# Kernel optimization log

Measured on AMD Instinct MI355X. Metric: run time of the kernel, lower is better.

## Reference

```python
import jax, jax.numpy as jnp
import numpy as np

N = 50000
E = 800000
IN, HID, OUT = 20, 64, 2
HEADS, HD = 4, 64
EPS = 1e-5


def setup_inputs() -> dict:
    key = jax.random.key(0)
    ks = jax.random.split(key, 24)
    rn = lambda k, shape, s=0.1: (jax.random.normal(k, shape, dtype=jnp.float32) * s)
    inp = {}
    inp['x'] = jax.random.normal(ks[0], (N, IN), dtype=jnp.float32)
    inp['edge_index'] = jax.random.randint(ks[1], (2, E), 0, N, dtype=jnp.int64)
    # SAGEConv1: lin_l (aggregated msgs, bias), lin_r (root, no bias)
    inp['Wl1'] = rn(ks[2], (IN, HID)); inp['Wr1'] = rn(ks[3], (IN, HID)); inp['b1'] = jnp.zeros((HID,), jnp.float32)
    inp['g1'] = jnp.ones((HID,), jnp.float32); inp['bt1'] = jnp.zeros((HID,), jnp.float32)
    # GATConv: W2 projects to heads*dim; att vectors per head; bias size HID (concat=False)
    inp['W2'] = rn(ks[4], (HID, HEADS * HD)); inp['att_src'] = rn(ks[5], (HEADS, HD)); inp['att_dst'] = rn(ks[6], (HEADS, HD)); inp['b2'] = jnp.zeros((HID,), jnp.float32)
    inp['g2'] = jnp.ones((HID,), jnp.float32); inp['bt2'] = jnp.zeros((HID,), jnp.float32)
    # SAGEConv3: hidden -> hidden//2
    inp['Wl3'] = rn(ks[7], (HID, HID // 2)); inp['Wr3'] = rn(ks[8], (HID, HID // 2)); inp['b3'] = jnp.zeros((HID // 2,), jnp.float32)
    inp['g3'] = jnp.ones((HID // 2,), jnp.float32); inp['bt3'] = jnp.zeros((HID // 2,), jnp.float32)
    # skip + classifier
    inp['Wskip'] = rn(ks[9], (IN, HID // 2)); inp['bskip'] = jnp.zeros((HID // 2,), jnp.float32)
    inp['Wc1'] = rn(ks[10], (HID // 2, 32)); inp['bc1'] = jnp.zeros((32,), jnp.float32)
    inp['Wc2'] = rn(ks[11], (32, OUT)); inp['bc2'] = jnp.zeros((OUT,), jnp.float32)
    return inp


def _bn_eval(h, g, b):
    # eval-mode BatchNorm with freshly initialized running stats (mean=0, var=1)
    return h * (g / jnp.sqrt(1.0 + EPS)) + b


def reference(x, edge_index, Wl1, Wr1, b1, g1, bt1, W2, att_src, att_dst, b2, g2, bt2,
              Wl3, Wr3, b3, g3, bt3, Wskip, bskip, Wc1, bc1, Wc2, bc2):
    src, dst = edge_index[0], edge_index[1]
    deg = jnp.clip(jax.ops.segment_sum(jnp.ones((E,), x.dtype), dst, num_segments=N), 1.0)

    def sage(h, Wl, Wr, b):
        agg = jax.ops.segment_sum(h[src], dst, num_segments=N) / deg[:, None]  # mean aggregation
        return agg @ Wl + h @ Wr + b

    def gat(h):
        hp = (h @ W2).reshape(N, HEADS, HD)                    # [N,H,D]
        a_s = jnp.einsum('nhd,hd->nh', hp, att_src)            # [N,H]
        a_d = jnp.einsum('nhd,hd->nh', hp, att_dst)
        e = jax.nn.leaky_relu(a_s[src] + a_d[dst], 0.2)        # [E,H]
        m = jax.ops.segment_max(e, dst, num_segments=N)        # segment softmax over incoming edges
        ex = jnp.exp(e - m[dst])
        denom = jax.ops.segment_sum(ex, dst, num_segments=N)
        alpha = ex / (denom[dst] + 1e-16)                      # [E,H]
        out = jax.ops.segment_sum(hp[src] * alpha[:, :, None], dst, num_segments=N)  # [N,H,D]
        return out.mean(axis=1) + b2                            # concat=False -> mean over heads

    identity = x @ Wskip + bskip
    h = jax.nn.relu(_bn_eval(sage(x, Wl1, Wr1, b1), g1, bt1))   # dropout inactive (eval)
    h = jax.nn.relu(_bn_eval(gat(h), g2, bt2))
    h = jax.nn.relu(_bn_eval(sage(h, Wl3, Wr3, b3), g3, bt3))
    h = h + identity
    logits = jax.nn.relu(h @ Wc1 + bc1) @ Wc2 + bc2
    return jax.nn.log_softmax(logits, axis=1)
```

## Files before the change

kernel.cpp:

```cpp
#include <hip/hip_runtime.h>
#include <hip/hip_fp16.h>
#include <math.h>

#define NN 50000
#define NE 800000
#define IN_F 20
#define HID 64
#define HEADS 4
#define HD 64
#define CH 32
#define C1 32
#define OUTC 2

__global__ void k_scan_block(const int* __restrict__ in, int* __restrict__ out,
                             int* __restrict__ bsum, int n){
  __shared__ int tmp[256];
  int g = blockIdx.x * 256 + threadIdx.x;
  int v = (g < n) ? in[g] : 0;
  tmp[threadIdx.x] = v;
  __syncthreads();
  for (int o = 1; o < 256; o <<= 1) {
    int t = ((int)threadIdx.x >= o) ? tmp[threadIdx.x - o] : 0;
    __syncthreads();
    tmp[threadIdx.x] += t;
    __syncthreads();
  }
  if (g < n) out[g] = tmp[threadIdx.x] - v;
  if (bsum && threadIdx.x == 255) bsum[blockIdx.x] = tmp[255];
}

__global__ void k_add_off(int* __restrict__ rowptr, const int* __restrict__ bsum_ex, int n){
  int g = blockIdx.x * 256 + threadIdx.x;
  if (g < n) rowptr[g] += bsum_ex[g >> 8];
  if (g == 0) rowptr[NN] = NE;
}

__global__ void k_scatter(const int* __restrict__ src, const int* __restrict__ dst,
                          const int* __restrict__ rowptr, int* __restrict__ cnt2,
                          unsigned* __restrict__ colu){
  int e = blockIdx.x * 256 + threadIdx.x;
  if (e >= NE) return;
  int d = dst[e];
  int p = rowptr[d] + atomicAdd(&cnt2[d], 1);
  colu[p] = (unsigned)src[e] | ((unsigned)d << 16);
}

__global__ void k_prep(const float* __restrict__ x, const float* __restrict__ W2,
                       const float* __restrict__ att_src, const float* __restrict__ att_dst,
                       const int* __restrict__ dst,
                       __half* __restrict__ xh, float* __restrict__ was,
                       float* __restrict__ wad, float* __restrict__ W2r,
                       int* __restrict__ count){
  int i = blockIdx.x * 256 + threadIdx.x;
  if (i < NN * IN_F) xh[i] = __float2half(x[i]);
  if (i < NE) atomicAdd(&count[dst[i]], 1);
  if (i < 256 * 64) {
    int hk = i >> 6, d = i & 63;
    int h = hk >> 6, k = hk & 63;
    W2r[i] = W2[k * 256 + h * 64 + d];
  }
  if (i < 256) {
    int h = i >> 6, k = i & 63;
    float s = 0.f, dd = 0.f;
    for (int d = 0; d < 64; d++) {
      float w = W2[k * 256 + h * 64 + d];
      s  += w * att_src[h * 64 + d];
      dd += w * att_dst[h * 64 + d];
    }
    was[i] = s; wad[i] = dd;
  }
}

__global__ void k_aggx_gather(const int* __restrict__ rowptr, const unsigned* __restrict__ colu,
                              const __half* __restrict__ xh, float* __restrict__ aggx){
  int wid = threadIdx.x >> 6, lane = threadIdx.x & 63;
  int grp = lane >> 5, f = lane & 31;
  int n = blockIdx.x * 4 + wid;
  if (n >= NN) return;
  int r0 = rowptr[n], r1 = rowptr[n + 1];
  int ff = f < IN_F ? f : 0;
  float acc = 0.f;
  int base = r0;
  for (; base + 8 <= r1; base += 8) {
    int s0 = colu[base + grp] & 0xffff;
    int s1 = colu[base + 2 + grp] & 0xffff;
    int s2 = colu[base + 4 + grp] & 0xffff;
    int s3 = colu[base + 6 + grp] & 0xffff;
    float v0 = __half2float(xh[s0 * IN_F + ff]);
    float v1 = __half2float(xh[s1 * IN_F + ff]);
    float v2 = __half2float(xh[s2 * IN_F + ff]);
    float v3 = __half2float(xh[s3 * IN_F + ff]);
    acc += (v0 + v1) + (v2 + v3);
  }
  for (int j = base + grp; j < r1; j += 2)
    acc += __half2float(xh[(colu[j] & 0xffff) * IN_F + ff]);
  acc += __shfl_xor(acc, 32);
  if (grp == 0 && f < IN_F) aggx[n * IN_F + f] = acc;
}

__global__ void k_sage1(const float* __restrict__ x, const float* __restrict__ aggx,
                        const int* __restrict__ count,
                        const float* __restrict__ Wl, const float* __restrict__ Wr,
                        const float* __restrict__ b, const float* __restrict__ g,
                        const float* __restrict__ bt,
                        const float* __restrict__ was, const float* __restrict__ wad,
                        __half* __restrict__ h1h, float* __restrict__ a_s,
                        float* __restrict__ a_d){
  __shared__ float sWl[IN_F * HID], sWr[IN_F * HID], sWas[256], sWad[256];
  for (int i = threadIdx.x; i < IN_F * HID; i += 256) { sWl[i] = Wl[i]; sWr[i] = Wr[i]; }
  { int i = threadIdx.x; sWas[i] = was[i]; sWad[i] = wad[i]; }
  __syncthreads();
  int idx = blockIdx.x * 256 + threadIdx.x;
  if (idx >= NN * HID) return;
  int n = idx >> 6, j = idx & 63;
  float inv = 1.f / fmaxf((float)count[n], 1.f);
  const float* xr = x + n * IN_F;
  const float* ar = aggx + n * IN_F;
  float acc = b[j];
  #pragma unroll
  for (int k = 0; k < IN_F; k++)
    acc += (ar[k] * inv) * sWl[k * HID + j] + xr[k] * sWr[k * HID + j];
  acc = acc * (g[j] * rsqrtf(1.f + 1e-5f)) + bt[j];
  acc = fmaxf(acc, 0.f);
  h1h[idx] = __float2half(acc);
  #pragma unroll
  for (int h = 0; h < HEADS; h++) {
    float vs = acc * sWas[h * 64 + j];
    float vd = acc * sWad[h * 64 + j];
    #pragma unroll
    for (int o = 32; o > 0; o >>= 1) { vs += __shfl_down(vs, o); vd += __shfl_down(vd, o); }
    if (j == 0) { a_s[n * 4 + h] = vs; a_d[n * 4 + h] = vd; }
  }
}

static __device__ __forceinline__ float4 edge_p(float4 as, float4 ad){
  float e0 = as.x + ad.x; e0 = e0 >= 0.f ? e0 : 0.2f * e0;
  float e1 = as.y + ad.y; e1 = e1 >= 0.f ? e1 : 0.2f * e1;
  float e2 = as.z + ad.z; e2 = e2 >= 0.f ? e2 : 0.2f * e2;
  float e3 = as.w + ad.w; e3 = e3 >= 0.f ? e3 : 0.2f * e3;
  return make_float4(__expf(e0), __expf(e1), __expf(e2), __expf(e3));
}

__global__ void k_gat_fused(const int* __restrict__ rowptr, const unsigned* __restrict__ colu,
                            const float4* __restrict__ a_s4, const float4* __restrict__ a_d4,
                            const __half* __restrict__ h1h, __half* __restrict__ z){
  int wid = threadIdx.x >> 6;
  int lane = threadIdx.x & 63;
  int grp = lane >> 5;
  int idx = lane & 31;
  int n = blockIdx.x * 4 + wid;
  if (n >= NN) return;
  int r0 = rowptr[n], r1 = rowptr[n + 1];
  float4 ad = a_d4[n];
  float l0 = 0.f, l1 = 0.f, l2 = 0.f, l3 = 0.f;
  float2 ac0 = {0,0}, ac1 = {0,0}, ac2 = {0,0}, ac3 = {0,0};
  int base = r0;
  for (; base + 8 <= r1; base += 8) {
    int s0 = colu[base + grp] & 0xffff;
    int s1 = colu[base + 2 + grp] & 0xffff;
    int s2 = colu[base + 4 + grp] & 0xffff;
    int s3 = colu[base + 6 + grp] & 0xffff;
    float4 as0 = a_s4[s0], as1 = a_s4[s1], as2 = a_s4[s2], as3 = a_s4[s3];
    float2 v0 = __half22float2(*(const __half2*)(h1h + (size_t)s0 * 64 + 2 * idx));
    float2 v1 = __half22float2(*(const __half2*)(h1h + (size_t)s1 * 64 + 2 * idx));
    float2 v2 = __half22float2(*(const __half2*)(h1h + (size_t)s2 * 64 + 2 * idx));
    float2 v3 = __half22float2(*(const __half2*)(h1h + (size_t)s3 * 64 + 2 * idx));
    float4 p0 = edge_p(as0, ad), p1 = edge_p(as1, ad);
    float4 p2 = edge_p(as2, ad), p3 = edge_p(as3, ad);
    l0 += (p0.x + p1.x) + (p2.x + p3.x);
    l1 += (p0.y + p1.y) + (p2.y + p3.y);
    l2 += (p0.z + p1.z) + (p2.z + p3.z);
    l3 += (p0.w + p1.w) + (p2.w + p3.w);
    ac0.x += p0.x*v0.x + p1.x*v1.x + p2.x*v2.x + p3.x*v3.x;
    ac0.y += p0.x*v0.y + p1.x*v1.y + p2.x*v2.y + p3.x*v3.y;
    ac1.x += p0.y*v0.x + p1.y*v1.x + p2.y*v2.x + p3.y*v3.x;
    ac1.y += p0.y*v0.y + p1.y*v1.y + p2.y*v2.y + p3.y*v3.y;
    ac2.x += p0.z*v0.x + p1.z*v1.x + p2.z*v2.x + p3.z*v3.x;
    ac2.y += p0.z*v0.y + p1.z*v1.y + p2.z*v2.y + p3.z*v3.y;
    ac3.x += p0.w*v0.x + p1.w*v1.x + p2.w*v2.x + p3.w*v3.x;
    ac3.y += p0.w*v0.y + p1.w*v1.y + p2.w*v2.y + p3.w*v3.y;
  }
  for (int j = base + grp; j < r1; j += 2) {
    int s = colu[j] & 0xffff;
    float4 p = edge_p(a_s4[s], ad);
    float2 v = __half22float2(*(const __half2*)(h1h + (size_t)s * 64 + 2 * idx));
    l0 += p.x; l1 += p.y; l2 += p.z; l3 += p.w;
    ac0.x += p.x*v.x; ac0.y += p.x*v.y;
    ac1.x += p.y*v.x; ac1.y += p.y*v.y;
    ac2.x += p.z*v.x; ac2.y += p.z*v.y;
    ac3.x += p.w*v.x; ac3.y += p.w*v.y;
  }
  l0 += __shfl_xor(l0, 32); l1 += __shfl_xor(l1, 32);
  l2 += __shfl_xor(l2, 32); l3 += __shfl_xor(l3, 32);
  ac0.x += __shfl_xor(ac0.x, 32); ac0.y += __shfl_xor(ac0.y, 32);
  ac1.x += __shfl_xor(ac1.x, 32); ac1.y += __shfl_xor(ac1.y, 32);
  ac2.x += __shfl_xor(ac2.x, 32); ac2.y += __shfl_xor(ac2.y, 32);
  ac3.x += __shfl_xor(ac3.x, 32); ac3.y += __shfl_xor(ac3.y, 32);
  if (grp == 0) {
    float i0 = 1.f / (4.f * (l0 + 1e-16f));
    float i1 = 1.f / (4.f * (l1 + 1e-16f));
    float i2 = 1.f / (4.f * (l2 + 1e-16f));
    float i3 = 1.f / (4.f * (l3 + 1e-16f));
    __half* zr = z + (size_t)n * 256;
    *(__half2*)(zr +       2 * idx) = __floats2half2_rn(ac0.x * i0, ac0.y * i0);
    *(__half2*)(zr +  64 + 2 * idx) = __floats2half2_rn(ac1.x * i1, ac1.y * i1);
    *(__half2*)(zr + 128 + 2 * idx) = __floats2half2_rn(ac2.x * i2, ac2.y * i2);
    *(__half2*)(zr + 192 + 2 * idx) = __floats2half2_rn(ac3.x * i3, ac3.y * i3);
  }
}

__global__ void __launch_bounds__(256) k_zproj(const __half* __restrict__ z,
                      const float* __restrict__ W2r, const float* __restrict__ b2,
                      const float* __restrict__ g2, const float* __restrict__ bt2,
                      float* __restrict__ h2, __half* __restrict__ h2h){
  __shared__ float sz[4][256];
  __shared__ float sacc[4][4][64];
  int tid = threadIdx.x;
  int w = tid >> 6, d = tid & 63;
  float wreg[64];
  #pragma unroll
  for (int i = 0; i < 64; i++) wreg[i] = W2r[(w * 64 + i) * 64 + d];
  float gd = g2[d] * rsqrtf(1.f + 1e-5f), btd = bt2[d], bd = b2[d];
  int n0base = blockIdx.x * 64;
  for (int r = 0; r < 16; r++) {
    int n0 = n0base + r * 4;
    for (int i = tid; i < 512; i += 256) {
      int m = i >> 7, c = (i & 127) * 2;
      int n = n0 + m;
      if (n < NN) {
        __half2 hv = *(const __half2*)(z + (size_t)n * 256 + c);
        float2 f = __half22float2(hv);
        sz[m][c] = f.x; sz[m][c + 1] = f.y;
      } else { sz[m][c] = 0.f; sz[m][c + 1] = 0.f; }
    }
    __syncthreads();
    #pragma unroll
    for (int m = 0; m < 4; m++) {
      float acc = 0.f;
      #pragma unroll
      for (int i = 0; i < 64; i++) acc += sz[m][w * 64 + i] * wreg[i];
      sacc[m][w][d] = acc;
    }
    __syncthreads();
    int n = n0 + w;
    if (n < NN) {
      float rr = sacc[w][0][d] + sacc[w][1][d] + sacc[w][2][d] + sacc[w][3][d] + bd;
      rr = rr * gd + btd;
      rr = fmaxf(rr, 0.f);
      h2[(size_t)n * 64 + d] = rr;
      h2h[(size_t)n * 64 + d] = __float2half(rr);
    }
    __syncthreads();
  }
}

__global__ void __launch_bounds__(256) k_sage3f(
    const int* __restrict__ rowptr, const unsigned* __restrict__ colu,
    const float* __restrict__ x, const float* __restrict__ h2,
    const __half* __restrict__ h2h, const int* __restrict__ count,
    const float* __restrict__ Wl3, const float* __restrict__ Wr3,
    const float* __restrict__ b3, const float* __restrict__ g3,
    const float* __restrict__ bt3, const float* __restrict__ Wskip,
    const float* __restrict__ bskip, float* __restrict__ h3){
  __shared__ float sWl[HID * CH], sWr[HID * CH], sWs[IN_F * CH];
  __shared__ float sA[4][HID], sH[4][HID];
  for (int i = threadIdx.x; i < HID * CH; i += 256) { sWl[i] = Wl3[i]; sWr[i] = Wr3[i]; }
  for (int i = threadIdx.x; i < IN_F * CH; i += 256) sWs[i] = Wskip[i];
  int wid = threadIdx.x >> 6, lane = threadIdx.x & 63;
  int grp = lane >> 5, idx = lane & 31;
  int n = blockIdx.x * 4 + wid;
  int nc = n < NN ? n : NN - 1;
  int r0 = rowptr[nc], r1 = rowptr[nc + 1];
  float2 av = {0, 0};
  int base = r0;
  for (; base + 8 <= r1; base += 8) {
    int s0 = colu[base + grp] & 0xffff;
    int s1 = colu[base + 2 + grp] & 0xffff;
    int s2 = colu[base + 4 + grp] & 0xffff;
    int s3 = colu[base + 6 + grp] & 0xffff;
    float2 v0 = __half22float2(*(const __half2*)(h2h + (size_t)s0 * 64 + 2 * idx));
    float2 v1 = __half22float2(*(const __half2*)(h2h + (size_t)s1 * 64 + 2 * idx));
    float2 v2 = __half22float2(*(const __half2*)(h2h + (size_t)s2 * 64 + 2 * idx));
    float2 v3 = __half22float2(*(const __half2*)(h2h + (size_t)s3 * 64 + 2 * idx));
    av.x += (v0.x + v1.x) + (v2.x + v3.x);
    av.y += (v0.y + v1.y) + (v2.y + v3.y);
  }
  for (int j = base + grp; j < r1; j += 2) {
    float2 v = __half22float2(*(const __half2*)(h2h + (size_t)(colu[j] & 0xffff) * 64 + 2 * idx));
    av.x += v.x; av.y += v.y;
  }
  av.x += __shfl_xor(av.x, 32);
  av.y += __shfl_xor(av.y, 32);
  float inv = 1.f / fmaxf((float)count[nc], 1.f);
  if (grp == 0) { sA[wid][2 * idx] = av.x * inv; sA[wid][2 * idx + 1] = av.y * inv; }
  sH[wid][lane] = h2[(size_t)nc * 64 + lane];
  __syncthreads();
  int kbase = grp * 32;
  float c0 = 0.f, c1 = 0.f;
  #pragma unroll
  for (int k0 = 0; k0 < 32; k0 += 2) {
    int k = kbase + k0;
    c0 += sA[wid][k] * sWl[k * CH + idx] + sH[wid][k] * sWr[k * CH + idx];
    c1 += sA[wid][k+1] * sWl[(k+1) * CH + idx] + sH[wid][k+1] * sWr[(k+1) * CH + idx];
  }
  float c = c0 + c1;
  c += __shfl_xor(c, 32);
  if (grp == 0 && n < NN) {
    float acc = c + b3[idx];
    acc = acc * (g3[idx] * rsqrtf(1.f + 1e-5f)) + bt3[idx];
    acc = fmaxf(acc, 0.f);
    float idn = bskip[idx];
    const float* xr = x + (size_t)n * IN_F;
    #pragma unroll
    for (int k = 0; k < IN_F; k++) idn += xr[k] * sWs[k * CH + idx];
    h3[(size_t)n * CH + idx] = acc + idn;
  }
}

__global__ void __launch_bounds__(256) k_cls(const float* __restrict__ h3,
                      const float* __restrict__ Wc1, const float* __restrict__ bc1,
                      const float* __restrict__ Wc2, const float* __restrict__ bc2,
                      float* __restrict__ out){
  __shared__ float sW1[C1 * C1], sW2[C1 * OUTC], sb1[C1], sb2[OUTC];
  __shared__ float sh3[256][CH + 1];
  int tid = threadIdx.x;
  int n0 = blockIdx.x * 256;
  for (int i = tid; i < C1 * C1; i += 256) sW1[i] = Wc1[i];
  if (tid < C1 * OUTC) sW2[tid] = Wc2[tid];
  if (tid < C1) sb1[tid] = bc1[tid];
  if (tid < OUTC) sb2[tid] = bc2[tid];
  for (int i = tid; i < 256 * CH; i += 256) {
    int m = i >> 5, c = i & 31;
    int n = n0 + m;
    sh3[m][c] = (n < NN) ? h3[(size_t)n * CH + c] : 0.f;
  }
  __syncthreads();
  int n = n0 + tid;
  if (n >= NN) return;
  float hrow[CH];
  #pragma unroll
  for (int j = 0; j < CH; j++) hrow[j] = sh3[tid][j];
  float l0 = sb2[0], l1 = sb2[1];
  #pragma unroll
  for (int i = 0; i < C1; i++) {
    float c0 = sb1[i], c1 = 0.f;
    #pragma unroll
    for (int j = 0; j < CH; j += 2) {
      c0 += hrow[j] * sW1[j * C1 + i];
      c1 += hrow[j + 1] * sW1[(j + 1) * C1 + i];
    }
    float c = fmaxf(c0 + c1, 0.f);
    l0 += c * sW2[i * OUTC + 0];
    l1 += c * sW2[i * OUTC + 1];
  }
  float mx = fmaxf(l0, l1);
  float lse = mx + logf(expf(l0 - mx) + expf(l1 - mx));
  out[n * OUTC + 0] = l0 - lse;
  out[n * OUTC + 1] = l1 - lse;
}

extern "C" void kernel_launch(void* const* d_in, const int* in_sizes, int n_in,
                              void* d_out, int out_size, void* d_ws, size_t ws_size,
                              hipStream_t stream) {
  const float* x       = (const float*)d_in[0];
  const int*   ei      = (const int*)d_in[1];
  const float* Wl1     = (const float*)d_in[2];
  const float* Wr1     = (const float*)d_in[3];
  const float* b1      = (const float*)d_in[4];
  const float* g1      = (const float*)d_in[5];
  const float* bt1     = (const float*)d_in[6];
  const float* W2      = (const float*)d_in[7];
  const float* att_src = (const float*)d_in[8];
  const float* att_dst = (const float*)d_in[9];
  const float* b2      = (const float*)d_in[10];
  const float* g2      = (const float*)d_in[11];
  const float* bt2     = (const float*)d_in[12];
  const float* Wl3     = (const float*)d_in[13];
  const float* Wr3     = (const float*)d_in[14];
  const float* b3      = (const float*)d_in[15];
  const float* g3      = (const float*)d_in[16];
  const float* bt3     = (const float*)d_in[17];
  const float* Wskip   = (const float*)d_in[18];
  const float* bskip   = (const float*)d_in[19];
  const float* Wc1     = (const float*)d_in[20];
  const float* bc1     = (const float*)d_in[21];
  const float* Wc2     = (const float*)d_in[22];
  const float* bc2     = (const float*)d_in[23];
  float* out = (float*)d_out;

  const int* src = ei;
  const int* dst = ei + NE;

  float* ws = (float*)d_ws;
  size_t off = 0;
  auto alloc = [&](size_t nf) { size_t o = off; off += (nf + 63) & ~(size_t)63; return o; };
  size_t o_count = alloc(NN);
  size_t o_cnt2  = alloc(NN);
  size_t zero_elems = off;
  size_t o_rowptr = alloc(NN + 1);
  size_t o_bsum   = alloc(256);
  size_t o_bsumex = alloc(256);
  size_t o_colu   = alloc(NE);
  size_t o_xh     = alloc((size_t)NN * IN_F / 2 + 64);
  size_t o_aggx   = alloc((size_t)NN * IN_F);
  size_t o_h1h    = alloc((size_t)NN * HID / 2 + 64);
  size_t o_as     = alloc((size_t)NN * HEADS);
  size_t o_ad     = alloc((size_t)NN * HEADS);
  size_t o_was    = alloc(256);
  size_t o_wad    = alloc(256);
  size_t o_w2r    = alloc(256 * 64);
  size_t o_z      = alloc((size_t)NN * 256 / 2 + 64);
  size_t o_h2     = alloc((size_t)NN * HID);
  size_t o_h2h    = alloc((size_t)NN * HID / 2 + 64);
  size_t o_h3     = alloc((size_t)NN * CH);
  (void)ws_size; (void)in_sizes; (void)n_in; (void)out_size;

  int* count     = (int*)(ws + o_count);
  int* cnt2      = (int*)(ws + o_cnt2);
  int* rowptr    = (int*)(ws + o_rowptr);
  int* bsum      = (int*)(ws + o_bsum);
  int* bsumex    = (int*)(ws + o_bsumex);
  unsigned* colu = (unsigned*)(ws + o_colu);
  __half* xh     = (__half*)(ws + o_xh);
  float* aggx    = ws + o_aggx;
  __half* h1h    = (__half*)(ws + o_h1h);
  float* a_s     = ws + o_as;
  float* a_d     = ws + o_ad;
  float* was     = ws + o_was;
  float* wad     = ws + o_wad;
  float* W2r     = ws + o_w2r;
  __half* z      = (__half*)(ws + o_z);
  float* h2      = ws + o_h2;
  __half* h2h    = (__half*)(ws + o_h2h);
  float* h3      = ws + o_h3;

  auto nb = [](long long n) { return (int)((n + 255) / 256); };
  const int nscan = nb(NN);

  hipMemsetAsync(ws, 0, zero_elems * sizeof(int), stream);
  k_prep<<<nb((long long)NN * IN_F), 256, 0, stream>>>(x, W2, att_src, att_dst, dst,
                                                       xh, was, wad, W2r, count);
  k_scan_block<<<nscan, 256, 0, stream>>>(count, rowptr, bsum, NN);
  k_scan_block<<<1, 256, 0, stream>>>(bsum, bsumex, nullptr, nscan);
  k_add_off<<<nscan, 256, 0, stream>>>(rowptr, bsumex, NN);
  k_scatter<<<nb(NE), 256, 0, stream>>>(src, dst, rowptr, cnt2, colu);
  k_aggx_gather<<<(NN + 3) / 4, 256, 0, stream>>>(rowptr, colu, xh, aggx);
  k_sage1<<<nb((long long)NN * HID), 256, 0, stream>>>(x, aggx, count, Wl1, Wr1, b1, g1, bt1,
                                                       was, wad, h1h, a_s, a_d);
  k_gat_fused<<<(NN + 3) / 4, 256, 0, stream>>>(rowptr, colu, (const float4*)a_s,
                                                (const float4*)a_d, h1h, z);
  k_zproj<<<(NN + 63) / 64, 256, 0, stream>>>(z, W2r, b2, g2, bt2, h2, h2h);
  k_sage3f<<<(NN + 3) / 4, 256, 0, stream>>>(rowptr, colu, x, h2, h2h, count,
                                             Wl3, Wr3, b3, g3, bt3, Wskip, bskip, h3);
  k_cls<<<(NN + 255) / 256, 256, 0, stream>>>(h3, Wc1, bc1, Wc2, bc2, out);
}
```

Baseline: 321.0 us.

## Split neighbor ranges per half-wave with prefetched indices; drop fp32 h2 and move skip to classifier

The three gather kernels now give each half-wave a contiguous half of the edge range instead of interleaved edges, and software-prefetch the next four column indices while the current four are processed. k_zproj no longer writes an fp32 copy of h2; k_sage3f reads the root features from the fp16 copy instead. The skip projection moves from k_sage3f into k_cls, which is one thread per node. This removes a full fp32 write and read of the hidden features and some per-warp work, at the cost of fp16 rounding on the root term and higher register use in the classifier.

```diff
diff --git a/kernel.cpp b/kernel.cpp
--- a/kernel.cpp
+++ b/kernel.cpp
@@ -78,22 +78,29 @@
   int n = blockIdx.x * 4 + wid;
   if (n >= NN) return;
   int r0 = rowptr[n], r1 = rowptr[n + 1];
+  int mid = r0 + ((r1 - r0) >> 1);
+  int jlo = grp ? mid : r0;
+  int jhi = grp ? r1 : mid;
   int ff = f < IN_F ? f : 0;
   float acc = 0.f;
-  int base = r0;
-  for (; base + 8 <= r1; base += 8) {
-    int s0 = colu[base + grp] & 0xffff;
-    int s1 = colu[base + 2 + grp] & 0xffff;
-    int s2 = colu[base + 4 + grp] & 0xffff;
-    int s3 = colu[base + 6 + grp] & 0xffff;
-    float v0 = __half2float(xh[s0 * IN_F + ff]);
-    float v1 = __half2float(xh[s1 * IN_F + ff]);
-    float v2 = __half2float(xh[s2 * IN_F + ff]);
-    float v3 = __half2float(xh[s3 * IN_F + ff]);
-    acc += (v0 + v1) + (v2 + v3);
-  }
-  for (int j = base + grp; j < r1; j += 2)
-    acc += __half2float(xh[(colu[j] & 0xffff) * IN_F + ff]);
+#define AX4(a,b,c,d) { \
+    float v0 = __half2float(xh[(int)((a)&0xffffu) * IN_F + ff]); \
+    float v1 = __half2float(xh[(int)((b)&0xffffu) * IN_F + ff]); \
+    float v2 = __half2float(xh[(int)((c)&0xffffu) * IN_F + ff]); \
+    float v3 = __half2float(xh[(int)((d)&0xffffu) * IN_F + ff]); \
+    acc += (v0 + v1) + (v2 + v3); }
+  int j = jlo;
+  if (j + 4 <= jhi) {
+    unsigned c0 = colu[j], c1 = colu[j+1], c2 = colu[j+2], c3 = colu[j+3];
+    for (j += 4; j + 4 <= jhi; j += 4) {
+      unsigned n0 = colu[j], n1 = colu[j+1], n2 = colu[j+2], n3 = colu[j+3];
+      AX4(c0, c1, c2, c3);
+      c0 = n0; c1 = n1; c2 = n2; c3 = n3;
+    }
+    AX4(c0, c1, c2, c3);
+  }
+  for (; j < jhi; j++) acc += __half2float(xh[(int)(colu[j] & 0xffffu) * IN_F + ff]);
+#undef AX4
   acc += __shfl_xor(acc, 32);
   if (grp == 0 && f < IN_F) aggx[n * IN_F + f] = acc;
 }
@@ -151,45 +158,56 @@
   int n = blockIdx.x * 4 + wid;
   if (n >= NN) return;
   int r0 = rowptr[n], r1 = rowptr[n + 1];
+  int mid = r0 + ((r1 - r0) >> 1);
+  int jlo = grp ? mid : r0;
+  int jhi = grp ? r1 : mid;
   float4 ad = a_d4[n];
   float l0 = 0.f, l1 = 0.f, l2 = 0.f, l3 = 0.f;
   float2 ac0 = {0,0}, ac1 = {0,0}, ac2 = {0,0}, ac3 = {0,0};
-  int base = r0;
-  for (; base + 8 <= r1; base += 8) {
-    int s0 = colu[base + grp] & 0xffff;
-    int s1 = colu[base + 2 + grp] & 0xffff;
-    int s2 = colu[base + 4 + grp] & 0xffff;
-    int s3 = colu[base + 6 + grp] & 0xffff;
-    float4 as0 = a_s4[s0], as1 = a_s4[s1], as2 = a_s4[s2], as3 = a_s4[s3];
-    float2 v0 = __half22float2(*(const __half2*)(h1h + (size_t)s0 * 64 + 2 * idx));
-    float2 v1 = __half22float2(*(const __half2*)(h1h + (size_t)s1 * 64 + 2 * idx));
-    float2 v2 = __half22float2(*(const __half2*)(h1h + (size_t)s2 * 64 + 2 * idx));
-    float2 v3 = __half22float2(*(const __half2*)(h1h + (size_t)s3 * 64 + 2 * idx));
-    float4 p0 = edge_p(as0, ad), p1 = edge_p(as1, ad);
-    float4 p2 = edge_p(as2, ad), p3 = edge_p(as3, ad);
-    l0 += (p0.x + p1.x) + (p2.x + p3.x);
-    l1 += (p0.y + p1.y) + (p2.y + p3.y);
-    l2 += (p0.z + p1.z) + (p2.z + p3.z);
-    l3 += (p0.w + p1.w) + (p2.w + p3.w);
-    ac0.x += p0.x*v0.x + p1.x*v1.x + p2.x*v2.x + p3.x*v3.x;
-    ac0.y += p0.x*v0.y + p1.x*v1.y + p2.x*v2.y + p3.x*v3.y;
-    ac1.x += p0.y*v0.x + p1.y*v1.x + p2.y*v2.x + p3.y*v3.x;
-    ac1.y += p0.y*v0.y + p1.y*v1.y + p2.y*v2.y + p3.y*v3.y;
-    ac2.x += p0.z*v0.x + p1.z*v1.x + p2.z*v2.x + p3.z*v3.x;
-    ac2.y += p0.z*v0.y + p1.z*v1.y + p2.z*v2.y + p3.z*v3.y;
-    ac3.x += p0.w*v0.x + p1.w*v1.x + p2.w*v2.x + p3.w*v3.x;
-    ac3.y += p0.w*v0.y + p1.w*v1.y + p2.w*v2.y + p3.w*v3.y;
-  }
-  for (int j = base + grp; j < r1; j += 2) {
-    int s = colu[j] & 0xffff;
-    float4 p = edge_p(a_s4[s], ad);
-    float2 v = __half22float2(*(const __half2*)(h1h + (size_t)s * 64 + 2 * idx));
-    l0 += p.x; l1 += p.y; l2 += p.z; l3 += p.w;
-    ac0.x += p.x*v.x; ac0.y += p.x*v.y;
-    ac1.x += p.y*v.x; ac1.y += p.y*v.y;
-    ac2.x += p.z*v.x; ac2.y += p.z*v.y;
-    ac3.x += p.w*v.x; ac3.y += p.w*v.y;
-  }
+#define GAT1(cc) { \
+    int s = (int)((cc) & 0xffffu); \
+    float4 as = a_s4[s]; \
+    float2 v = __half22float2(*(const __half2*)(h1h + (size_t)s * 64 + 2 * idx)); \
+    float4 p = edge_p(as, ad); \
+    l0 += p.x; l1 += p.y; l2 += p.z; l3 += p.w; \
+    ac0.x += p.x*v.x; ac0.y += p.x*v.y; \
+    ac1.x += p.y*v.x; ac1.y += p.y*v.y; \
+    ac2.x += p.z*v.x; ac2.y += p.z*v.y; \
+    ac3.x += p.w*v.x; ac3.y += p.w*v.y; }
+#define GAT4(q0,q1,q2,q3) { \
+    int s0=(int)((q0)&0xffffu), s1=(int)((q1)&0xffffu), s2=(int)((q2)&0xffffu), s3=(int)((q3)&0xffffu); \
+    float4 as0 = a_s4[s0], as1 = a_s4[s1], as2 = a_s4[s2], as3 = a_s4[s3]; \
+    float2 v0 = __half22float2(*(const __half2*)(h1h + (size_t)s0 * 64 + 2 * idx)); \
+    float2 v1 = __half22float2(*(const __half2*)(h1h + (size_t)s1 * 64 + 2 * idx)); \
+    float2 v2 = __half22float2(*(const __half2*)(h1h + (size_t)s2 * 64 + 2 * idx)); \
+    float2 v3 = __half22float2(*(const __half2*)(h1h + (size_t)s3 * 64 + 2 * idx)); \
+    float4 p0 = edge_p(as0, ad), p1 = edge_p(as1, ad); \
+    float4 p2 = edge_p(as2, ad), p3 = edge_p(as3, ad); \
+    l0 += (p0.x + p1.x) + (p2.x + p3.x); \
+    l1 += (p0.y + p1.y) + (p2.y + p3.y); \
+    l2 += (p0.z + p1.z) + (p2.z + p3.z); \
+    l3 += (p0.w + p1.w) + (p2.w + p3.w); \
+    ac0.x += p0.x*v0.x + p1.x*v1.x + p2.x*v2.x + p3.x*v3.x; \
+    ac0.y += p0.x*v0.y + p1.x*v1.y + p2.x*v2.y + p3.x*v3.y; \
+    ac1.x += p0.y*v0.x + p1.y*v1.x + p2.y*v2.x + p3.y*v3.x; \
+    ac1.y += p0.y*v0.y + p1.y*v1.y + p2.y*v2.y + p3.y*v3.y; \
+    ac2.x += p0.z*v0.x + p1.z*v1.x + p2.z*v2.x + p3.z*v3.x; \
+    ac2.y += p0.z*v0.y + p1.z*v1.y + p2.z*v2.y + p3.z*v3.y; \
+    ac3.x += p0.w*v0.x + p1.w*v1.x + p2.w*v2.x + p3.w*v3.x; \
+    ac3.y += p0.w*v0.y + p1.w*v1.y + p2.w*v2.y + p3.w*v3.y; }
+  int j = jlo;
+  if (j + 4 <= jhi) {
+    unsigned c0 = colu[j], c1 = colu[j+1], c2 = colu[j+2], c3 = colu[j+3];
+    for (j += 4; j + 4 <= jhi; j += 4) {
+      unsigned n0 = colu[j], n1 = colu[j+1], n2 = colu[j+2], n3 = colu[j+3];
+      GAT4(c0, c1, c2, c3);
+      c0 = n0; c1 = n1; c2 = n2; c3 = n3;
+    }
+    GAT4(c0, c1, c2, c3);
+  }
+  for (; j < jhi; j++) { unsigned cc = colu[j]; GAT1(cc); }
+#undef GAT4
+#undef GAT1
   l0 += __shfl_xor(l0, 32); l1 += __shfl_xor(l1, 32);
   l2 += __shfl_xor(l2, 32); l3 += __shfl_xor(l3, 32);
   ac0.x += __shfl_xor(ac0.x, 32); ac0.y += __shfl_xor(ac0.y, 32);
@@ -212,7 +230,7 @@
 __global__ void __launch_bounds__(256) k_zproj(const __half* __restrict__ z,
                       const float* __restrict__ W2r, const float* __restrict__ b2,
                       const float* __restrict__ g2, const float* __restrict__ bt2,
-                      float* __restrict__ h2, __half* __restrict__ h2h){
+                      __half* __restrict__ h2h){
   __shared__ float sz[4][256];
   __shared__ float sacc[4][4][64];
   int tid = threadIdx.x;
@@ -247,7 +265,6 @@
       float rr = sacc[w][0][d] + sacc[w][1][d] + sacc[w][2][d] + sacc[w][3][d] + bd;
       rr = rr * gd + btd;
       rr = fmaxf(rr, 0.f);
-      h2[(size_t)n * 64 + d] = rr;
       h2h[(size_t)n * 64 + d] = __float2half(rr);
     }
     __syncthreads();
@@ -256,44 +273,50 @@
 
 __global__ void __launch_bounds__(256) k_sage3f(
     const int* __restrict__ rowptr, const unsigned* __restrict__ colu,
-    const float* __restrict__ x, const float* __restrict__ h2,
     const __half* __restrict__ h2h, const int* __restrict__ count,
     const float* __restrict__ Wl3, const float* __restrict__ Wr3,
     const float* __restrict__ b3, const float* __restrict__ g3,
-    const float* __restrict__ bt3, const float* __restrict__ Wskip,
-    const float* __restrict__ bskip, float* __restrict__ h3){
-  __shared__ float sWl[HID * CH], sWr[HID * CH], sWs[IN_F * CH];
+    const float* __restrict__ bt3, float* __restrict__ h3){
+  __shared__ float sWl[HID * CH], sWr[HID * CH];
   __shared__ float sA[4][HID], sH[4][HID];
   for (int i = threadIdx.x; i < HID * CH; i += 256) { sWl[i] = Wl3[i]; sWr[i] = Wr3[i]; }
-  for (int i = threadIdx.x; i < IN_F * CH; i += 256) sWs[i] = Wskip[i];
   int wid = threadIdx.x >> 6, lane = threadIdx.x & 63;
   int grp = lane >> 5, idx = lane & 31;
   int n = blockIdx.x * 4 + wid;
   int nc = n < NN ? n : NN - 1;
   int r0 = rowptr[nc], r1 = rowptr[nc + 1];
+  int mid = r0 + ((r1 - r0) >> 1);
+  int jlo = grp ? mid : r0;
+  int jhi = grp ? r1 : mid;
   float2 av = {0, 0};
-  int base = r0;
-  for (; base + 8 <= r1; base += 8) {
-    int s0 = colu[base + grp] & 0xffff;
-    int s1 = colu[base + 2 + grp] & 0xffff;
-    int s2 = colu[base + 4 + grp] & 0xffff;
-    int s3 = colu[base + 6 + grp] & 0xffff;
-    float2 v0 = __half22float2(*(const __half2*)(h2h + (size_t)s0 * 64 + 2 * idx));
-    float2 v1 = __half22float2(*(const __half2*)(h2h + (size_t)s1 * 64 + 2 * idx));
-    float2 v2 = __half22float2(*(const __half2*)(h2h + (size_t)s2 * 64 + 2 * idx));
-    float2 v3 = __half22float2(*(const __half2*)(h2h + (size_t)s3 * 64 + 2 * idx));
-    av.x += (v0.x + v1.x) + (v2.x + v3.x);
-    av.y += (v0.y + v1.y) + (v2.y + v3.y);
-  }
-  for (int j = base + grp; j < r1; j += 2) {
-    float2 v = __half22float2(*(const __half2*)(h2h + (size_t)(colu[j] & 0xffff) * 64 + 2 * idx));
+#define AGG4(q0,q1,q2,q3) { \
+    int s0=(int)((q0)&0xffffu), s1=(int)((q1)&0xffffu), s2=(int)((q2)&0xffffu), s3=(int)((q3)&0xffffu); \
+    float2 v0 = __half22float2(*(const __half2*)(h2h + (size_t)s0 * 64 + 2 * idx)); \
+    float2 v1 = __half22float2(*(const __half2*)(h2h + (size_t)s1 * 64 + 2 * idx)); \
+    float2 v2 = __half22float2(*(const __half2*)(h2h + (size_t)s2 * 64 + 2 * idx)); \
+    float2 v3 = __half22float2(*(const __half2*)(h2h + (size_t)s3 * 64 + 2 * idx)); \
+    av.x += (v0.x + v1.x) + (v2.x + v3.x); \
+    av.y += (v0.y + v1.y) + (v2.y + v3.y); }
+  int j = jlo;
+  if (j + 4 <= jhi) {
+    unsigned c0 = colu[j], c1 = colu[j+1], c2 = colu[j+2], c3 = colu[j+3];
+    for (j += 4; j + 4 <= jhi; j += 4) {
+      unsigned n0 = colu[j], n1 = colu[j+1], n2 = colu[j+2], n3 = colu[j+3];
+      AGG4(c0, c1, c2, c3);
+      c0 = n0; c1 = n1; c2 = n2; c3 = n3;
+    }
+    AGG4(c0, c1, c2, c3);
+  }
+  for (; j < jhi; j++) {
+    float2 v = __half22float2(*(const __half2*)(h2h + (size_t)(colu[j] & 0xffffu) * 64 + 2 * idx));
     av.x += v.x; av.y += v.y;
   }
+#undef AGG4
   av.x += __shfl_xor(av.x, 32);
   av.y += __shfl_xor(av.y, 32);
   float inv = 1.f / fmaxf((float)count[nc], 1.f);
   if (grp == 0) { sA[wid][2 * idx] = av.x * inv; sA[wid][2 * idx + 1] = av.y * inv; }
-  sH[wid][lane] = h2[(size_t)nc * 64 + lane];
+  sH[wid][lane] = __half2float(h2h[(size_t)nc * 64 + lane]);
   __syncthreads();
   int kbase = grp * 32;
   float c0 = 0.f, c1 = 0.f;
@@ -308,26 +331,25 @@
   if (grp == 0 && n < NN) {
     float acc = c + b3[idx];
     acc = acc * (g3[idx] * rsqrtf(1.f + 1e-5f)) + bt3[idx];
-    acc = fmaxf(acc, 0.f);
-    float idn = bskip[idx];
-    const float* xr = x + (size_t)n * IN_F;
-    #pragma unroll
-    for (int k = 0; k < IN_F; k++) idn += xr[k] * sWs[k * CH + idx];
-    h3[(size_t)n * CH + idx] = acc + idn;
+    h3[(size_t)n * CH + idx] = fmaxf(acc, 0.f);
   }
 }
 
 __global__ void __launch_bounds__(256) k_cls(const float* __restrict__ h3,
+                      const float* __restrict__ x,
+                      const float* __restrict__ Wskip, const float* __restrict__ bskip,
                       const float* __restrict__ Wc1, const float* __restrict__ bc1,
                       const float* __restrict__ Wc2, const float* __restrict__ bc2,
                       float* __restrict__ out){
   __shared__ float sW1[C1 * C1], sW2[C1 * OUTC], sb1[C1], sb2[OUTC];
+  __shared__ float sWs[IN_F * CH], sbsk[CH];
   __shared__ float sh3[256][CH + 1];
   int tid = threadIdx.x;
   int n0 = blockIdx.x * 256;
   for (int i = tid; i < C1 * C1; i += 256) sW1[i] = Wc1[i];
+  for (int i = tid; i < IN_F * CH; i += 256) sWs[i] = Wskip[i];
   if (tid < C1 * OUTC) sW2[tid] = Wc2[tid];
-  if (tid < C1) sb1[tid] = bc1[tid];
+  if (tid < C1) { sb1[tid] = bc1[tid]; sbsk[tid] = bskip[tid]; }
   if (tid < OUTC) sb2[tid] = bc2[tid];
   for (int i = tid; i < 256 * CH; i += 256) {
     int m = i >> 5, c = i & 31;
@@ -337,9 +359,17 @@
   __syncthreads();
   int n = n0 + tid;
   if (n >= NN) return;
+  float xr[IN_F];
+  #pragma unroll
+  for (int k = 0; k < IN_F; k++) xr[k] = x[(size_t)n * IN_F + k];
   float hrow[CH];
   #pragma unroll
-  for (int j = 0; j < CH; j++) hrow[j] = sh3[tid][j];
+  for (int j = 0; j < CH; j++) {
+    float idn = sbsk[j];
+    #pragma unroll
+    for (int k = 0; k < IN_F; k++) idn += xr[k] * sWs[k * CH + j];
+    hrow[j] = sh3[tid][j] + idn;
+  }
   float l0 = sb2[0], l1 = sb2[1];
   #pragma unroll
   for (int i = 0; i < C1; i++) {
@@ -410,7 +440,6 @@
   size_t o_wad    = alloc(256);
   size_t o_w2r    = alloc(256 * 64);
   size_t o_z      = alloc((size_t)NN * 256 / 2 + 64);
-  size_t o_h2     = alloc((size_t)NN * HID);
   size_t o_h2h    = alloc((size_t)NN * HID / 2 + 64);
   size_t o_h3     = alloc((size_t)NN * CH);
   (void)ws_size; (void)in_sizes; (void)n_in; (void)out_size;
@@ -430,7 +459,6 @@
   float* wad     = ws + o_wad;
   float* W2r     = ws + o_w2r;
   __half* z      = (__half*)(ws + o_z);
-  float* h2      = ws + o_h2;
   __half* h2h    = (__half*)(ws + o_h2h);
   float* h3      = ws + o_h3;
 
@@ -449,8 +477,8 @@
                                                        was, wad, h1h, a_s, a_d);
   k_gat_fused<<<(NN + 3) / 4, 256, 0, stream>>>(rowptr, colu, (const float4*)a_s,
                                                 (const float4*)a_d, h1h, z);
-  k_zproj<<<(NN + 63) / 64, 256, 0, stream>>>(z, W2r, b2, g2, bt2, h2, h2h);
-  k_sage3f<<<(NN + 3) / 4, 256, 0, stream>>>(rowptr, colu, x, h2, h2h, count,
-                                             Wl3, Wr3, b3, g3, bt3, Wskip, bskip, h3);
-  k_cls<<<(NN + 255) / 256, 256, 0, stream>>>(h3, Wc1, bc1, Wc2, bc2, out);
-}
+  k_zproj<<<(NN + 63) / 64, 256, 0, stream>>>(z, W2r, b2, g2, bt2, h2h);
+  k_sage3f<<<(NN + 3) / 4, 256, 0, stream>>>(rowptr, colu, h2h, count,
+                                             Wl3, Wr3, b3, g3, bt3, h3);
+  k_cls<<<(NN + 255) / 256, 256, 0, stream>>>(h3, x, Wskip, bskip, Wc1, bc1, Wc2, bc2, out);
+}
```

New measurement: 309.9 us. -3.4%, faster.
